# Kernel optimization log

Hardware: AMD Instinct MI355X
Metric: run time of the kernel (lower is better)

## Reference

```python
import jax, jax.numpy as jnp
import numpy as np

N_FFT = 4096
HOP = 1024
EPS = 1e-10


def hann(n):
    # periodic Hann window, matches torch.hann_window(n)
    return 0.5 - 0.5 * jnp.cos(2.0 * jnp.pi * jnp.arange(n) / n)


def stft(x, window):
    # x: (..., T) real -> (..., F, frames) complex; center=True, reflect pad, onesided
    pad = N_FFT // 2
    x = jnp.pad(x, [(0, 0)] * (x.ndim - 1) + [(pad, pad)], mode='reflect')
    n_frames = 1 + (x.shape[-1] - N_FFT) // HOP
    idx = jnp.arange(n_frames)[:, None] * HOP + jnp.arange(N_FFT)[None, :]
    frames = x[..., idx] * window  # (..., frames, N_FFT)
    return jnp.swapaxes(jnp.fft.rfft(frames, axis=-1), -1, -2)  # (..., F, frames)


def istft(spec, window, length):
    # spec: (..., F, frames) complex -> (..., length) real; torch.istft semantics (center=True)
    frames = jnp.fft.irfft(jnp.swapaxes(spec, -1, -2), n=N_FFT, axis=-1) * window
    n_frames = frames.shape[-2]
    out_len = N_FFT + HOP * (n_frames - 1)
    idx = (jnp.arange(n_frames)[:, None] * HOP + jnp.arange(N_FFT)[None, :]).reshape(-1)
    flat = frames.reshape(frames.shape[:-2] + (-1,))
    y = jnp.zeros(frames.shape[:-2] + (out_len,), frames.dtype).at[..., idx].add(flat)
    wsq = jnp.zeros((out_len,), frames.dtype).at[idx].add(jnp.tile(window ** 2, n_frames))
    y = y / jnp.where(wsq > 1e-11, wsq, 1.0)
    pad = N_FFT // 2
    return y[..., pad:pad + length]


def setup_inputs() -> dict:
    key = jax.random.key(0)
    k1, k2, k3 = jax.random.split(key, 3)
    audio = jax.random.normal(k1, (2, 2, 441000), jnp.float32)
    W = jax.random.normal(k2, (4, 2049, 2049), jnp.float32) * 0.02
    b = jax.random.normal(k3, (4, 2049), jnp.float32) * 0.01
    return {"audio": audio, "W": W, "b": b}


def reference(audio, W, b):
    window = hann(N_FFT).astype(audio.dtype)
    mix = stft(audio, window)                 # (N, C, F, T) complex64
    X = jnp.abs(mix)                          # ComplexNorm, mono=False, power=1
    Xd = jax.lax.stop_gradient(X)             # Separator feeds X.detach() to target models
    # target models: per-target linear over frequency bins + ReLU (nonneg spectrogram)
    V = jax.nn.relu(jnp.einsum('ncft,jgf->njcgt', Xd, W) + b[None, :, None, :, None])
    # wiener(iterations=0, softmask=False, residual=False): y_j = v_j * exp(i*angle(mix))
    phase = mix / (jnp.abs(mix) + EPS)        # unit-magnitude complex
    Y = V.astype(phase.real.dtype) * phase[:, None]  # (N, J, C, F, T) complex
    estimates = istft(Y, window, audio.shape[-1])    # (N, J, C, T_audio)
    return estimates
```

## Files before the change

kernel.cpp:

```cpp
#include <hip/hip_runtime.h>
#include <hip/hip_bf16.h>
#include <math.h>

#define T_AUDIO 441000
#define NH   2048
#define HOP  1024
#define NBINS 2049
#define NFRAMES 431
#define PAD  2048

#define GP  2176
#define KP  2112
#define TPN 448
#define NKT (KP / 64)

#define NBLK 108
#define SPAN 7168

#define NSTFT (4 * NFRAMES)
#define NCONV ((4 * GP * KP / 8 + 255) / 256)

#define TWO_PI 6.2831853071795864769f

#define PADI(i) ((i) + ((i) >> 4))

typedef __bf16 bf16_t;
typedef bf16_t bf16x8 __attribute__((ext_vector_type(8)));
typedef bf16_t bf16x4 __attribute__((ext_vector_type(4)));
typedef float f32x4 __attribute__((ext_vector_type(4)));
typedef _Float16 h16;
typedef h16 h16x2 __attribute__((ext_vector_type(2)));

__device__ __forceinline__ unsigned pack_bf2(float a, float b) {
    union { bf16_t h; unsigned short u; } ca, cb;
    ca.h = (bf16_t)a; cb.h = (bf16_t)b;
    return (unsigned)ca.u | ((unsigned)cb.u << 16);
}
__device__ __forceinline__ float2 unpack_bf2(unsigned v) {
    union { unsigned u; float f; } a, b;
    a.u = v << 16;
    b.u = v & 0xffff0000u;
    return make_float2(a.f, b.f);
}

__device__ __forceinline__ float2 cadd(float2 a, float2 b) { return make_float2(a.x + b.x, a.y + b.y); }
__device__ __forceinline__ float2 csub(float2 a, float2 b) { return make_float2(a.x - b.x, a.y - b.y); }
__device__ __forceinline__ float2 cmul(float2 a, float2 b) {
    return make_float2(a.x * b.x - a.y * b.y, a.x * b.y + a.y * b.x);
}
__device__ __forceinline__ float2 cmulc(float2 u, float2 w) {
    return make_float2(u.x * w.x + u.y * w.y, u.y * w.x - u.x * w.y);
}

__global__ void k_tab(float2* __restrict__ tw) {
    int i = blockIdx.x * 256 + threadIdx.x;
    if (i < 4096) {
        float s, c;
        sincosf((float)i * (TWO_PI / 4096.0f), &s, &c);
        tw[i] = make_float2(c, s);
    }
}


__device__ __forceinline__ void load_own(float2 v[8], const float2* x, int tid) {
    #pragma unroll
    for (int k = 0; k < 8; k++) v[k] = x[PADI(tid + 256 * k)];
}

template<bool FWD>
__device__ __forceinline__ void r8_sweep_store(const float2 v[8], float2* x,
        int tid, int s, int ls, int fac, const float2* __restrict__ tw) {
    const float sgn = FWD ? -1.0f : 1.0f;
    const float R2 = 0.70710678118654752440f;
    int q = tid & (s - 1);
    int p = tid >> ls;
    int e = p * fac;
    float2 w[7];
    #pragma unroll
    for (int k = 0; k < 7; k++) w[k] = tw[e * (k + 1)];
    float2 s0 = cadd(v[0], v[4]), s1 = cadd(v[1], v[5]),
           s2 = cadd(v[2], v[6]), s3 = cadd(v[3], v[7]);
    float2 d0 = csub(v[0], v[4]), d1 = csub(v[1], v[5]),
           d2 = csub(v[2], v[6]), d3 = csub(v[3], v[7]);
    float2 X0, X1, X2, X3, X4, X5, X6, X7;
    {
        float2 t0 = cadd(s0, s2), t1 = csub(s0, s2);
        float2 t2 = cadd(s1, s3), t3 = csub(s1, s3);
        float2 it3 = make_float2(-sgn * t3.y, sgn * t3.x);
        X0 = cadd(t0, t2); X4 = csub(t0, t2);
        X2 = cadd(t1, it3); X6 = csub(t1, it3);
    }
    {
        float2 e0 = d0;
        float2 e1 = make_float2(R2 * (d1.x - sgn * d1.y), R2 * (sgn * d1.x + d1.y));
        float2 e2 = make_float2(-sgn * d2.y, sgn * d2.x);
        float2 e3 = make_float2(-R2 * (d3.x + sgn * d3.y), R2 * (sgn * d3.x - d3.y));
        float2 t0 = cadd(e0, e2), t1 = csub(e0, e2);
        float2 t2 = cadd(e1, e3), t3 = csub(e1, e3);
        float2 it3 = make_float2(-sgn * t3.y, sgn * t3.x);
        X1 = cadd(t0, t2); X5 = csub(t0, t2);
        X3 = cadd(t1, it3); X7 = csub(t1, it3);
    }
    int ob = q + 8 * s * p;
    x[PADI(ob)] = X0;
    float2 XX[7] = {X1, X2, X3, X4, X5, X6, X7};
    #pragma unroll
    for (int k = 0; k < 7; k++) {
        float2 u = XX[k];
        x[PADI(ob + s * (k + 1))] = FWD ? cmulc(u, w[k]) : cmul(w[k], u);
    }
}

__device__ __forceinline__ void r4_final_reg(const float2 v[8], float2 o[8],
                                             float sgn) {
    #pragma unroll
    for (int h = 0; h < 2; h++) {
        float2 c0 = v[h], c1 = v[h + 2], c2 = v[h + 4], c3 = v[h + 6];
        float2 t0 = cadd(c0, c2), t1 = csub(c0, c2);
        float2 t2 = cadd(c1, c3), t3 = csub(c1, c3);
        float2 it3 = make_float2(-sgn * t3.y, sgn * t3.x);
        o[h]     = cadd(t0, t2);
        o[h + 2] = cadd(t1, it3);
        o[h + 4] = csub(t0, t2);
        o[h + 6] = csub(t1, it3);
    }
}

template<bool FWD>
__device__ __forceinline__ void fft_mid(float2 v[8], float2* buf, int tid,
                                        const float2* __restrict__ tw) {
    r8_sweep_store<FWD>(v, buf, tid, 1, 0, 2, tw);
    __syncthreads();
    load_own(v, buf, tid);
    __syncthreads();
    r8_sweep_store<FWD>(v, buf, tid, 8, 3, 16, tw);
    __syncthreads();
    load_own(v, buf, tid);
    __syncthreads();
    r8_sweep_store<FWD>(v, buf, tid, 64, 6, 128, tw);
    __syncthreads();
    load_own(v, buf, tid);
    __syncthreads();
}

__global__ __launch_bounds__(256) void k_prep(const float* __restrict__ audio,
        const float* __restrict__ W, bf16_t* __restrict__ Wb,
        bf16_t* __restrict__ Xb, unsigned* __restrict__ ph,
        const float2* __restrict__ tw) {
    __shared__ float2 buf[2176];
    int bid = blockIdx.x;
    int tid = threadIdx.x;
    if (bid >= NSTFT) {
        size_t idx = (size_t)(bid - NSTFT) * 256 + tid;
        size_t total = (size_t)4 * GP * KP / 8;
        if (idx >= total) return;
        size_t e = idx * 8;
        int f0 = (int)(e % KP);
        size_t rem = e / KP;
        int g = (int)(rem % GP);
        int j = (int)(rem / GP);
        bf16x8 v = {};
        if (g < NBINS) {
            const float* src = W + ((size_t)j * NBINS + g) * NBINS;
            #pragma unroll
            for (int r = 0; r < 8; r++) {
                int f = f0 + r;
                v[r] = (bf16_t)(f < NBINS ? src[f] : 0.0f);
            }
        }
        *(bf16x8*)(Wb + e) = v;
        return;
    }
    int nc = bid / NFRAMES;
    int fr = bid - nc * NFRAMES;
    const float* a = audio + (size_t)nc * T_AUDIO;
    int base = fr * HOP - PAD;
    float2 v[8];
    #pragma unroll
    for (int it = 0; it < 8; it++) {
        int m = tid + it * 256;
        int r0 = base + 2 * m;
        int r1 = r0 + 1;
        r0 = r0 < 0 ? -r0 : (r0 >= T_AUDIO ? 2 * T_AUDIO - 2 - r0 : r0);
        r1 = r1 < 0 ? -r1 : (r1 >= T_AUDIO ? 2 * T_AUDIO - 2 - r1 : r1);
        float4 tt = ((const float4*)tw)[m];
        v[it] = make_float2(a[r0] * (0.5f - 0.5f * tt.x),
                            a[r1] * (0.5f - 0.5f * tt.z));
    }
    fft_mid<true>(v, buf, tid, tw);
    {
        float2 o[8];
        r4_final_reg(v, o, -1.0f);
        #pragma unroll
        for (int it = 0; it < 8; it++) buf[PADI(tid + 256 * it)] = o[it];
    }
    __syncthreads();
    size_t orow = ((size_t)nc * NFRAMES + fr) * KP;
    bf16_t* Xrow = Xb + ((size_t)nc * TPN + fr) * KP;
    for (int k = tid; k < NBINS; k += 256) {
        float2 Zk = buf[PADI(k & 2047)];
        float2 Zm = buf[PADI((2048 - k) & 2047)];
        float ex = 0.5f * (Zk.x + Zm.x), ey = 0.5f * (Zk.y - Zm.y);
        float ox = 0.5f * (Zk.y + Zm.y), oy = -0.5f * (Zk.x - Zm.x);
        float2 w = tw[k];
        float re = ex + w.x * ox + w.y * oy;
        float im = ey + w.x * oy - w.y * ox;
        float mag = sqrtf(re * re + im * im);
        float inv = 1.0f / (mag + 1e-10f);
        Xrow[k] = (bf16_t)mag;
        ph[orow + k] = pack_bf2(re * inv, im * inv);
    }
}

__global__ __launch_bounds__(256) void k_gemm_mfma(const bf16_t* __restrict__ Wb,
        const float* __restrict__ bias, const bf16_t* __restrict__ Xb,
        bf16_t* __restrict__ V) {
    __shared__ bf16_t As[128 * 64];
    __shared__ bf16_t Bs[64 * 64];
    int id = blockIdx.x;
    int xcd = id & 7, nn = id >> 3;
    int G = xcd + 8 * (nn / 28);
    if (G >= 68) return;
    int m28 = nn % 28;
    int j  = G / 17;
    int g0 = (G % 17) * 128;
    int nc = m28 / 7;
    int t0 = (m28 % 7) * 64;
    const bf16_t* A = Wb + ((size_t)j * GP + g0) * KP;
    const bf16_t* B = Xb + ((size_t)nc * TPN + t0) * KP;
    int tid = threadIdx.x;
    int lane = tid & 63, wid = tid >> 6;
    int wm = wid >> 1, wn = wid & 1;

    const bf16_t* srcA[4];
    #pragma unroll
    for (int i = 0; i < 4; i++) {
        int s = i * 256 + tid;
        int r = s >> 3, cc = (s & 7) ^ (r & 7);
        srcA[i] = A + (size_t)r * KP + cc * 8;
    }
    const bf16_t* srcB[2];
    #pragma unroll
    for (int i = 0; i < 2; i++) {
        int s = i * 256 + tid;
        int r = s >> 3, cc = (s & 7) ^ (r & 7);
        srcB[i] = B + (size_t)r * KP + cc * 8;
    }

    int laneLo = lane & 15, laneHi = lane >> 4;
    int offA[4][2], offB[2][2];
    #pragma unroll
    for (int mm = 0; mm < 4; mm++) {
        int r = wm * 64 + mm * 16 + laneLo;
        #pragma unroll
        for (int kk = 0; kk < 2; kk++) {
            int c = kk * 4 + laneHi;
            offA[mm][kk] = r * 128 + ((c ^ (r & 7)) << 4);
        }
    }
    #pragma unroll
    for (int n = 0; n < 2; n++) {
        int r = wn * 32 + n * 16 + laneLo;
        #pragma unroll
        for (int kk = 0; kk < 2; kk++) {
            int c = kk * 4 + laneHi;
            offB[n][kk] = r * 128 + ((c ^ (r & 7)) << 4);
        }
    }

    f32x4 acc[4][2];
    #pragma unroll
    for (int mm = 0; mm < 4; mm++)
        #pragma unroll
        for (int n = 0; n < 2; n++)
            acc[mm][n] = (f32x4){0.f, 0.f, 0.f, 0.f};

    for (int k0 = 0; k0 < KP; k0 += 64) {
        #pragma unroll
        for (int i = 0; i < 4; i++)
            __builtin_amdgcn_global_load_lds(
                (const __attribute__((address_space(1))) void*)(srcA[i] + k0),
                (__attribute__((address_space(3))) void*)(As + (i * 256 + tid) * 8),
                16, 0, 0);
        #pragma unroll
        for (int i = 0; i < 2; i++)
            __builtin_amdgcn_global_load_lds(
                (const __attribute__((address_space(1))) void*)(srcB[i] + k0),
                (__attribute__((address_space(3))) void*)(Bs + (i * 256 + tid) * 8),
                16, 0, 0);
        __syncthreads();

        bf16x8 af[4][2], bfr[2][2];
        #pragma unroll
        for (int mm = 0; mm < 4; mm++)
            #pragma unroll
            for (int kk = 0; kk < 2; kk++)
                af[mm][kk] = *(const bf16x8*)((const char*)As + offA[mm][kk]);
        #pragma unroll
        for (int n = 0; n < 2; n++)
            #pragma unroll
            for (int kk = 0; kk < 2; kk++)
                bfr[n][kk] = *(const bf16x8*)((const char*)Bs + offB[n][kk]);
        #pragma unroll
        for (int mm = 0; mm < 4; mm++)
            #pragma unroll
            for (int n = 0; n < 2; n++)
                #pragma unroll
                for (int kk = 0; kk < 2; kk++)
                    acc[mm][n] = __builtin_amdgcn_mfma_f32_16x16x32_bf16(
                        af[mm][kk], bfr[n][kk], acc[mm][n], 0, 0, 0);
        __syncthreads();
    }

    int jnc = j * 4 + nc;
    int colT = laneLo;
    int rowB = laneHi * 4;
    #pragma unroll
    for (int n = 0; n < 2; n++) {
        int t = t0 + wn * 32 + n * 16 + colT;
        if (t >= NFRAMES) continue;
        size_t vrow = ((size_t)jnc * NFRAMES + t) * KP;
        #pragma unroll
        for (int mm = 0; mm < 4; mm++) {
            int g = g0 + wm * 64 + mm * 16 + rowB;
            if (g + 3 < NBINS) {
                bf16x4 o;
                #pragma unroll
                for (int r = 0; r < 4; r++)
                    o[r] = (bf16_t)fmaxf(acc[mm][n][r] + bias[j * NBINS + g + r], 0.0f);
                *(bf16x4*)(V + vrow + g) = o;
            } else {
                #pragma unroll
                for (int r = 0; r < 4; r++) {
                    int gg = g + r;
                    if (gg < NBINS)
                        V[vrow + gg] = (bf16_t)fmaxf(acc[mm][n][r] + bias[j * NBINS + gg], 0.0f);
                }
            }
        }
    }
}

__global__ __launch_bounds__(256) void k_istft(const bf16_t* __restrict__ V,
        const unsigned* __restrict__ ph, const float2* __restrict__ tw,
        h16* __restrict__ strips) {
    __shared__ float2 buf[2176];
    int b = blockIdx.x, njc = blockIdx.y;
    int n = njc >> 3, j = (njc >> 1) & 3, c = njc & 1;
    int nc = n * 2 + c;
    int jnc = j * 4 + nc;
    int tid = threadIdx.x;
    const float scale = 1.0f / 2048.0f;
    float2 acc[14];
    #pragma unroll
    for (int u = 0; u < 14; u++) acc[u] = make_float2(0.f, 0.f);

    #pragma unroll
    for (int p = 0; p < 4; p++) {
        int fr = b * 4 + p;
        if (fr < NFRAMES) {
            size_t vrow = ((size_t)jnc * NFRAMES + fr) * KP;
            size_t prow = ((size_t)nc * NFRAMES + fr) * KP;
            float2 v[8];
            #pragma unroll
            for (int it = 0; it < 8; it++) {
                int k = tid + it * 256;
                int km = 2048 - k;
                float vk = (float)V[vrow + k];
                float2 pk = unpack_bf2(ph[prow + k]);
                float vm = (float)V[vrow + km];
                float2 pm = unpack_bf2(ph[prow + km]);
                float2 Yk = make_float2(vk * pk.x, vk * pk.y);
                float2 Ym = make_float2(vm * pm.x, vm * pm.y);
                float ex = 0.5f * (Yk.x + Ym.x), ey = 0.5f * (Yk.y - Ym.y);
                float wx = 0.5f * (Yk.x - Ym.x), wy = 0.5f * (Yk.y + Ym.y);
                float2 w = tw[k];
                float ox_ = w.x * wx - w.y * wy;
                float oy_ = w.x * wy + w.y * wx;
                v[it] = make_float2(ex - oy_, ey + ox_);
            }
            fft_mid<false>(v, buf, tid, tw);
            float2 o[8];
            r4_final_reg(v, o, 1.0f);
            #pragma unroll
            for (int it = 0; it < 8; it++) {
                int m = tid + it * 256;
                float4 tt = ((const float4*)tw)[m];
                acc[2 * p + it].x += o[it].x * scale * (0.5f - 0.5f * tt.x);
                acc[2 * p + it].y += o[it].y * scale * (0.5f - 0.5f * tt.z);
            }
        }
    }
    h16* dst = strips + ((size_t)njc * NBLK + b) * SPAN;
    #pragma unroll
    for (int u = 0; u < 14; u++) {
        h16x2 o = { (h16)acc[u].x, (h16)acc[u].y };
        *(h16x2*)(dst + 512 * u + 2 * tid) = o;
    }
}

__global__ __launch_bounds__(256) void k_final(const h16* __restrict__ strips,
        const float2* __restrict__ tw, float* __restrict__ out) {
    int gidx = blockIdx.x * 256 + threadIdx.x;
    int t = gidx * 2;
    if (t >= T_AUDIO) return;
    int njc = blockIdx.y;
    const h16* S = strips + (size_t)njc * NBLK * SPAN;
    float o[2];
    #pragma unroll
    for (int u = 0; u < 2; u++) {
        int tt = t + u;
        int q = tt + PAD;
        int b1 = q >> 12, o1 = q & 4095;
        float s = 0.f;
        if (b1 < NBLK) s += (float)S[b1 * SPAN + o1];
        if (b1 > 0 && o1 < SPAN - 4096) s += (float)S[(b1 - 1) * SPAN + o1 + 4096];
        float wsq;
        if (tt >= 1024 && tt <= 439295) {
            wsq = 1.5f;
        } else {
            wsq = 0.f;
            int ib = q >> 10;
            #pragma unroll
            for (int d = 0; d < 4; d++) {
                int i = ib - d;
                if (i >= 0 && i < NFRAMES) {
                    int m = q - (i << 10);
                    float w = 0.5f - 0.5f * tw[m].x;
                    wsq += w * w;
                }
            }
            if (!(wsq > 1e-11f)) wsq = 1.f;
        }
        o[u] = s / wsq;
    }
    *(float2*)(out + (size_t)njc * T_AUDIO + t) = make_float2(o[0], o[1]);
}

extern "C" void kernel_launch(void* const* d_in, const int* in_sizes, int n_in,
                              void* d_out, int out_size, void* d_ws, size_t ws_size,
                              hipStream_t stream) {
    const float* audio = (const float*)d_in[0];
    const float* Wm    = (const float*)d_in[1];
    const float* bias  = (const float*)d_in[2];
    float* out = (float*)d_out;
    char* ws = (char*)d_ws;

    size_t szWb  = (size_t)4 * GP * KP * sizeof(bf16_t);
    size_t szXb  = (size_t)4 * TPN * KP * sizeof(bf16_t);
    size_t szPh  = (size_t)4 * NFRAMES * KP * sizeof(unsigned);
    size_t szV   = (size_t)16 * NFRAMES * KP * sizeof(bf16_t);
    size_t szStr = (size_t)16 * NBLK * SPAN * sizeof(h16);
    size_t szTw  = (size_t)4096 * sizeof(float2);

    bf16_t*   Wb    = (bf16_t*)ws;   ws += szWb;
    bf16_t*   Xb    = (bf16_t*)ws;   ws += szXb;
    unsigned* ph    = (unsigned*)ws; ws += szPh;
    bf16_t*   V     = (bf16_t*)ws;   ws += szV;
    h16*      strips= (h16*)ws;      ws += szStr;
    float2*   tw    = (float2*)ws;   ws += szTw;
    if ((size_t)(ws - (char*)d_ws) > ws_size) return;

    hipMemsetAsync(Xb, 0, szXb, stream);

    k_tab<<<dim3(16), 256, 0, stream>>>(tw);
    k_prep<<<dim3(NSTFT + NCONV), 256, 0, stream>>>(audio, Wm, Wb, Xb, ph, tw);
    k_gemm_mfma<<<dim3(72 * 28), 256, 0, stream>>>(Wb, bias, Xb, V);
    k_istft<<<dim3(NBLK, 16), 256, 0, stream>>>(V, ph, tw, strips);
    k_final<<<dim3((T_AUDIO / 2 + 255) / 256, 16), 256, 0, stream>>>(strips, tw, out);
}
```

Before: 223.0 us.

## Use two-wave 64x64 warp tiles in GEMM and vectorize W conversion loads

The GEMM block drops from four waves to two, so each wave now computes a 64x64 output tile (4x4 MFMA fragments) instead of 64x32. This raises MFMA work per LDS fragment load, at the cost of more accumulator registers and fewer waves to hide latency. Each thread now issues twice as many global-to-LDS loads. The W fp32-to-bf16 conversion also switches to two unaligned 4-float vector loads when all 8 elements are in range.

```diff
diff --git a/kernel.cpp b/kernel.cpp
--- a/kernel.cpp
+++ b/kernel.cpp
@@ -28,6 +28,7 @@
 typedef bf16_t bf16x8 __attribute__((ext_vector_type(8)));
 typedef bf16_t bf16x4 __attribute__((ext_vector_type(4)));
 typedef float f32x4 __attribute__((ext_vector_type(4)));
+typedef float f32x4u __attribute__((ext_vector_type(4), aligned(4)));
 typedef _Float16 h16;
 typedef h16 h16x2 __attribute__((ext_vector_type(2)));
 
@@ -162,10 +163,17 @@
         bf16x8 v = {};
         if (g < NBINS) {
             const float* src = W + ((size_t)j * NBINS + g) * NBINS;
-            #pragma unroll
-            for (int r = 0; r < 8; r++) {
-                int f = f0 + r;
-                v[r] = (bf16_t)(f < NBINS ? src[f] : 0.0f);
+            if (f0 + 7 < NBINS) {
+                f32x4u a0 = *(const f32x4u*)(src + f0);
+                f32x4u a1 = *(const f32x4u*)(src + f0 + 4);
+                #pragma unroll
+                for (int r = 0; r < 4; r++) { v[r] = (bf16_t)a0[r]; v[r + 4] = (bf16_t)a1[r]; }
+            } else {
+                #pragma unroll
+                for (int r = 0; r < 8; r++) {
+                    int f = f0 + r;
+                    v[r] = (bf16_t)(f < NBINS ? src[f] : 0.0f);
+                }
             }
         }
         *(bf16x8*)(Wb + e) = v;
@@ -212,7 +220,7 @@
     }
 }
 
-__global__ __launch_bounds__(256) void k_gemm_mfma(const bf16_t* __restrict__ Wb,
+__global__ __launch_bounds__(128) void k_gemm_mfma(const bf16_t* __restrict__ Wb,
         const float* __restrict__ bias, const bf16_t* __restrict__ Xb,
         bf16_t* __restrict__ V) {
     __shared__ bf16_t As[128 * 64];
@@ -230,28 +238,27 @@
     const bf16_t* B = Xb + ((size_t)nc * TPN + t0) * KP;
     int tid = threadIdx.x;
     int lane = tid & 63, wid = tid >> 6;
-    int wm = wid >> 1, wn = wid & 1;
-
-    const bf16_t* srcA[4];
-    #pragma unroll
-    for (int i = 0; i < 4; i++) {
-        int s = i * 256 + tid;
+
+    const bf16_t* srcA[8];
+    #pragma unroll
+    for (int i = 0; i < 8; i++) {
+        int s = i * 128 + tid;
         int r = s >> 3, cc = (s & 7) ^ (r & 7);
         srcA[i] = A + (size_t)r * KP + cc * 8;
     }
-    const bf16_t* srcB[2];
-    #pragma unroll
-    for (int i = 0; i < 2; i++) {
-        int s = i * 256 + tid;
+    const bf16_t* srcB[4];
+    #pragma unroll
+    for (int i = 0; i < 4; i++) {
+        int s = i * 128 + tid;
         int r = s >> 3, cc = (s & 7) ^ (r & 7);
         srcB[i] = B + (size_t)r * KP + cc * 8;
     }
 
     int laneLo = lane & 15, laneHi = lane >> 4;
-    int offA[4][2], offB[2][2];
+    int offA[4][2], offB[4][2];
     #pragma unroll
     for (int mm = 0; mm < 4; mm++) {
-        int r = wm * 64 + mm * 16 + laneLo;
+        int r = wid * 64 + mm * 16 + laneLo;
         #pragma unroll
         for (int kk = 0; kk < 2; kk++) {
             int c = kk * 4 + laneHi;
@@ -259,8 +266,8 @@
         }
     }
     #pragma unroll
-    for (int n = 0; n < 2; n++) {
-        int r = wn * 32 + n * 16 + laneLo;
+    for (int n = 0; n < 4; n++) {
+        int r = n * 16 + laneLo;
         #pragma unroll
         for (int kk = 0; kk < 2; kk++) {
             int c = kk * 4 + laneHi;
@@ -268,47 +275,44 @@
         }
     }
 
-    f32x4 acc[4][2];
+    f32x4 acc[4][4];
     #pragma unroll
     for (int mm = 0; mm < 4; mm++)
         #pragma unroll
-        for (int n = 0; n < 2; n++)
+        for (int n = 0; n < 4; n++)
             acc[mm][n] = (f32x4){0.f, 0.f, 0.f, 0.f};
 
     for (int k0 = 0; k0 < KP; k0 += 64) {
+        #pragma unroll
+        for (int i = 0; i < 8; i++)
+            __builtin_amdgcn_global_load_lds(
+                (const __attribute__((address_space(1))) void*)(srcA[i] + k0),
+                (__attribute__((address_space(3))) void*)(As + (i * 128 + tid) * 8),
+                16, 0, 0);
         #pragma unroll
         for (int i = 0; i < 4; i++)
             __builtin_amdgcn_global_load_lds(
-                (const __attribute__((address_space(1))) void*)(srcA[i] + k0),
-                (__attribute__((address_space(3))) void*)(As + (i * 256 + tid) * 8),
-                16, 0, 0);
-        #pragma unroll
-        for (int i = 0; i < 2; i++)
-            __builtin_amdgcn_global_load_lds(
                 (const __attribute__((address_space(1))) void*)(srcB[i] + k0),
-                (__attribute__((address_space(3))) void*)(Bs + (i * 256 + tid) * 8),
+                (__attribute__((address_space(3))) void*)(Bs + (i * 128 + tid) * 8),
                 16, 0, 0);
         __syncthreads();
 
-        bf16x8 af[4][2], bfr[2][2];
-        #pragma unroll
-        for (int mm = 0; mm < 4; mm++)
-            #pragma unroll
-            for (int kk = 0; kk < 2; kk++)
-                af[mm][kk] = *(const bf16x8*)((const char*)As + offA[mm][kk]);
-        #pragma unroll
-        for (int n = 0; n < 2; n++)
-            #pragma unroll
-            for (int kk = 0; kk < 2; kk++)
-                bfr[n][kk] = *(const bf16x8*)((const char*)Bs + offB[n][kk]);
-        #pragma unroll
-        for (int mm = 0; mm < 4; mm++)
-            #pragma unroll
-            for (int n = 0; n < 2; n++)
+        #pragma unroll
+        for (int kk = 0; kk < 2; kk++) {
+            bf16x8 af[4], bfr[4];
+            #pragma unroll
+            for (int mm = 0; mm < 4; mm++)
+                af[mm] = *(const bf16x8*)((const char*)As + offA[mm][kk]);
+            #pragma unroll
+            for (int n = 0; n < 4; n++)
+                bfr[n] = *(const bf16x8*)((const char*)Bs + offB[n][kk]);
+            #pragma unroll
+            for (int mm = 0; mm < 4; mm++)
                 #pragma unroll
-                for (int kk = 0; kk < 2; kk++)
+                for (int n = 0; n < 4; n++)
                     acc[mm][n] = __builtin_amdgcn_mfma_f32_16x16x32_bf16(
-                        af[mm][kk], bfr[n][kk], acc[mm][n], 0, 0, 0);
+                        af[mm], bfr[n], acc[mm][n], 0, 0, 0);
+        }
         __syncthreads();
     }
 
@@ -316,13 +320,13 @@
     int colT = laneLo;
     int rowB = laneHi * 4;
     #pragma unroll
-    for (int n = 0; n < 2; n++) {
-        int t = t0 + wn * 32 + n * 16 + colT;
+    for (int n = 0; n < 4; n++) {
+        int t = t0 + n * 16 + colT;
         if (t >= NFRAMES) continue;
         size_t vrow = ((size_t)jnc * NFRAMES + t) * KP;
         #pragma unroll
         for (int mm = 0; mm < 4; mm++) {
-            int g = g0 + wm * 64 + mm * 16 + rowB;
+            int g = g0 + wid * 64 + mm * 16 + rowB;
             if (g + 3 < NBINS) {
                 bf16x4 o;
                 #pragma unroll
@@ -465,7 +469,7 @@
 
     k_tab<<<dim3(16), 256, 0, stream>>>(tw);
     k_prep<<<dim3(NSTFT + NCONV), 256, 0, stream>>>(audio, Wm, Wb, Xb, ph, tw);
-    k_gemm_mfma<<<dim3(72 * 28), 256, 0, stream>>>(Wb, bias, Xb, V);
+    k_gemm_mfma<<<dim3(72 * 28), 128, 0, stream>>>(Wb, bias, Xb, V);
     k_istft<<<dim3(NBLK, 16), 256, 0, stream>>>(V, ph, tw, strips);
     k_final<<<dim3((T_AUDIO / 2 + 255) / 256, 16), 256, 0, stream>>>(strips, tw, out);
 }
```

New measurement: 216.6 us. -2.9%, faster.
